# Kernel optimization log

Measured on AMD Instinct MI355X. Metric: run time of the kernel, lower is better.

Reference implementation:

```python
import jax, jax.numpy as jnp
import numpy as np

TEMPERATURE = 1.0  # forward default
INIT_STD = 0.01    # per-class gate init: N(0, 0.01)

def setup_inputs() -> dict:
    key = jax.random.key(0)
    kf, kws, kw1, kw2 = jax.random.split(key, 4)
    B, F, H, C, E = 256, 2048, 512, 512, 8
    Hh = H // 2  # 256
    features = jax.random.normal(kf, (B, F), dtype=jnp.float32)
    # shared transform Linear(F, H) -- default torch init approximated by small normal
    Ws = jax.random.normal(kws, (F, H), dtype=jnp.float32) * (1.0 / np.sqrt(F))
    bs = jnp.zeros((H,), dtype=jnp.float32)
    # per-class gates, stacked over class dim: N(0, 0.01) init, zero bias (as in module)
    W1 = jax.random.normal(kw1, (C, H, Hh), dtype=jnp.float32) * INIT_STD
    b1 = jnp.zeros((C, Hh), dtype=jnp.float32)
    W2 = jax.random.normal(kw2, (C, Hh, E), dtype=jnp.float32) * INIT_STD
    b2 = jnp.zeros((C, E), dtype=jnp.float32)
    return {"features": features, "Ws": Ws, "bs": bs, "W1": W1, "b1": b1, "W2": W2, "b2": b2}

def reference(features, Ws, bs, W1, b1, W2, b2):
    # shared transform: Linear -> ReLU (Dropout is identity at inference)
    shared = jax.nn.relu(features @ Ws + bs)                      # [B, H]
    # batched per-class MLP: one grouped GEMM across all classes
    h = jax.nn.relu(jnp.einsum('bh,chk->bck', shared, W1) + b1)   # [B, C, H/2]
    gate_logits = jnp.einsum('bck,cke->bce', h, W2) + b2          # [B, C, E]
    gate_weights = jax.nn.softmax(gate_logits / TEMPERATURE, axis=-1)
    return (gate_weights, gate_logits)
```

## Files before the change

### kernel.cpp

```cpp
#include <hip/hip_runtime.h>
#include <hip/hip_bf16.h>

#define BATCH 256
#define F_DIM 2048
#define H_DIM 512
#define HH    256
#define NCLS  512
#define E_DIM 8

typedef __attribute__((ext_vector_type(8))) short  bf16x8;
typedef __attribute__((ext_vector_type(4))) float  f32x4;
typedef __attribute__((ext_vector_type(4))) unsigned short u16x4;

__device__ __forceinline__ unsigned short f2bf(float x) {
    union { float f; unsigned int u; } v; v.f = x;
    unsigned int r = v.u + 0x7fffu + ((v.u >> 16) & 1u);
    return (unsigned short)(r >> 16);
}

__global__ __launch_bounds__(256) void k_gemm1(
    const float* __restrict__ features,
    const float* __restrict__ Ws,
    float* __restrict__ partials)
{
    const int tid = threadIdx.x;
    const int lane = tid & 63;
    const int wave = tid >> 6;
    const int job = blockIdx.x * 4 + wave;
    const int kidx = job & 7;
    const int ng  = (job >> 3) & 7;
    const int mt  = job >> 6;
    const int l15 = lane & 15, quad = lane >> 4;
    const int m0 = mt * 16, n0 = ng * 64, kb = kidx * 256;

    f32x4 z = {0.f, 0.f, 0.f, 0.f};
    f32x4 acc[4];
#pragma unroll
    for (int nf = 0; nf < 4; ++nf) acc[nf] = z;

#pragma unroll
    for (int ks = 0; ks < 8; ++ks) {
        const int kk = kb + ks * 32 + quad * 8;
        f32x4 a0 = *(const f32x4*)(features + (size_t)(m0 + l15) * F_DIM + kk);
        f32x4 a1 = *(const f32x4*)(features + (size_t)(m0 + l15) * F_DIM + kk + 4);
        bf16x8 aF;
#pragma unroll
        for (int j = 0; j < 4; ++j) { aF[j] = (short)f2bf(a0[j]); aF[4 + j] = (short)f2bf(a1[j]); }
#pragma unroll
        for (int nf = 0; nf < 4; ++nf) {
            bf16x8 bF;
#pragma unroll
            for (int j = 0; j < 8; ++j)
                bF[j] = (short)f2bf(Ws[(size_t)(kk + j) * H_DIM + n0 + nf * 16 + l15]);
            acc[nf] = __builtin_amdgcn_mfma_f32_16x16x32_bf16(aF, bF, acc[nf], 0, 0, 0);
        }
    }
    float* po = partials + (size_t)kidx * (BATCH * H_DIM);
#pragma unroll
    for (int nf = 0; nf < 4; ++nf)
#pragma unroll
        for (int r = 0; r < 4; ++r)
            po[(size_t)(m0 + quad * 4 + r) * H_DIM + n0 + nf * 16 + l15] = acc[nf][r];
}

__global__ __launch_bounds__(256) void k_reduce_relu(
    const float* __restrict__ partials, const float* __restrict__ bs,
    unsigned short* __restrict__ sharedA)
{
    const int idx = (blockIdx.x * 256 + threadIdx.x) * 4;
    f32x4 s = *(const f32x4*)(partials + idx);
#pragma unroll
    for (int p = 1; p < 8; ++p)
        s += *(const f32x4*)(partials + (size_t)p * (BATCH * H_DIM) + idx);
    s += *(const f32x4*)(bs + (idx & (H_DIM - 1)));
    u16x4 o;
#pragma unroll
    for (int j = 0; j < 4; ++j) {
        float v = s[j] > 0.f ? s[j] : 0.f;
        o[j] = f2bf(v);
    }
    *(u16x4*)(sharedA + idx) = o;
}

__global__ __launch_bounds__(512) void k_main(
    const unsigned short* __restrict__ sharedA,
    const float* __restrict__ W1,
    const float* __restrict__ b1,
    const float* __restrict__ W2,
    const float* __restrict__ b2,
    float* __restrict__ out)
{
    const int c = blockIdx.x;
    const int tid = threadIdx.x;
    const int lane = tid & 63;
    const int wave = tid >> 6;
    const int l15 = lane & 15;
    const int quad = lane >> 4;
    const int g  = wave & 3;
    const int mh = wave >> 2;
    const int n0w = g * 64;
    const int m0w = mh * 128;

    const float* __restrict__ W1c = W1 + (size_t)c * (H_DIM * HH);

    __shared__ float slot[4][BATCH][E_DIM];

    f32x4 z = {0.f, 0.f, 0.f, 0.f};
    f32x4 acc[8][4];
#pragma unroll
    for (int mf = 0; mf < 8; ++mf)
#pragma unroll
        for (int nf = 0; nf < 4; ++nf) acc[mf][nf] = z;

    float braw[2][32];
#pragma unroll
    for (int nf = 0; nf < 4; ++nf)
#pragma unroll
        for (int j = 0; j < 8; ++j)
            braw[0][nf * 8 + j] = W1c[(size_t)(quad * 8 + j) * HH + n0w + nf * 16 + l15];

#pragma unroll
    for (int ks = 0; ks < 16; ++ks) {
        const int cur = ks & 1;
        if (ks < 15) {
            const int k0n = (ks + 1) * 32;
#pragma unroll
            for (int nf = 0; nf < 4; ++nf)
#pragma unroll
                for (int j = 0; j < 8; ++j)
                    braw[cur ^ 1][nf * 8 + j] =
                        W1c[(size_t)(k0n + quad * 8 + j) * HH + n0w + nf * 16 + l15];
        }
        bf16x8 bF[4];
#pragma unroll
        for (int nf = 0; nf < 4; ++nf)
#pragma unroll
            for (int j = 0; j < 8; ++j)
                bF[nf][j] = (short)f2bf(braw[cur][nf * 8 + j]);

        const int k0 = ks * 32 + quad * 8;
#pragma unroll
        for (int mf = 0; mf < 8; ++mf) {
            bf16x8 aF = *(const bf16x8*)(sharedA + (size_t)(m0w + mf * 16 + l15) * H_DIM + k0);
#pragma unroll
            for (int nf = 0; nf < 4; ++nf)
                acc[mf][nf] = __builtin_amdgcn_mfma_f32_16x16x32_bf16(aF, bF[nf], acc[mf][nf], 0, 0, 0);
        }
    }

    float b1v[4];
    f32x4 w2a[4], w2b[4];
#pragma unroll
    for (int nf = 0; nf < 4; ++nf) {
        const int col = n0w + nf * 16 + l15;
        b1v[nf] = b1[(size_t)c * HH + col];
        w2a[nf] = *(const f32x4*)(W2 + ((size_t)c * HH + col) * E_DIM);
        w2b[nf] = *(const f32x4*)(W2 + ((size_t)c * HH + col) * E_DIM + 4);
    }

#pragma unroll
    for (int mf = 0; mf < 8; ++mf) {
        float part[4][E_DIM];
#pragma unroll
        for (int r = 0; r < 4; ++r)
#pragma unroll
            for (int e = 0; e < E_DIM; ++e) part[r][e] = 0.f;
#pragma unroll
        for (int nf = 0; nf < 4; ++nf) {
#pragma unroll
            for (int r = 0; r < 4; ++r) {
                float h = acc[mf][nf][r] + b1v[nf];
                h = h > 0.f ? h : 0.f;
                part[r][0] += h * w2a[nf][0]; part[r][1] += h * w2a[nf][1];
                part[r][2] += h * w2a[nf][2]; part[r][3] += h * w2a[nf][3];
                part[r][4] += h * w2b[nf][0]; part[r][5] += h * w2b[nf][1];
                part[r][6] += h * w2b[nf][2]; part[r][7] += h * w2b[nf][3];
            }
        }
#pragma unroll
        for (int r = 0; r < 4; ++r)
#pragma unroll
            for (int e = 0; e < E_DIM; ++e) {
                float v = part[r][e];
                v += __shfl_xor(v, 1, 16);
                v += __shfl_xor(v, 2, 16);
                v += __shfl_xor(v, 4, 16);
                v += __shfl_xor(v, 8, 16);
                part[r][e] = v;
            }
        if (l15 == 0) {
#pragma unroll
            for (int r = 0; r < 4; ++r) {
                const int row = m0w + mf * 16 + quad * 4 + r;
                f32x4 lo = {part[r][0], part[r][1], part[r][2], part[r][3]};
                f32x4 hi = {part[r][4], part[r][5], part[r][6], part[r][7]};
                *(f32x4*)(&slot[g][row][0]) = lo;
                *(f32x4*)(&slot[g][row][4]) = hi;
            }
        }
    }
    __syncthreads();

    if (tid < BATCH) {
        f32x4 lg0 = *(f32x4*)(&slot[0][tid][0]);
        f32x4 lg1 = *(f32x4*)(&slot[0][tid][4]);
#pragma unroll
        for (int s = 1; s < 4; ++s) {
            lg0 += *(f32x4*)(&slot[s][tid][0]);
            lg1 += *(f32x4*)(&slot[s][tid][4]);
        }
        lg0 += *(const f32x4*)(b2 + (size_t)c * E_DIM);
        lg1 += *(const f32x4*)(b2 + (size_t)c * E_DIM + 4);

        float lg[8] = {lg0[0], lg0[1], lg0[2], lg0[3], lg1[0], lg1[1], lg1[2], lg1[3]};
        float mx = lg[0];
#pragma unroll
        for (int e = 1; e < 8; ++e) mx = lg[e] > mx ? lg[e] : mx;
        float ex[8], s = 0.f;
#pragma unroll
        for (int e = 0; e < 8; ++e) { ex[e] = __expf(lg[e] - mx); s += ex[e]; }
        const float inv = 1.f / s;

        const size_t ob = ((size_t)tid * NCLS + c) * E_DIM;
        f32x4 w0 = {ex[0] * inv, ex[1] * inv, ex[2] * inv, ex[3] * inv};
        f32x4 w1 = {ex[4] * inv, ex[5] * inv, ex[6] * inv, ex[7] * inv};
        *(f32x4*)(out + ob) = w0;
        *(f32x4*)(out + ob + 4) = w1;
        const size_t lbase = (size_t)BATCH * NCLS * E_DIM;
        f32x4 o0 = {lg[0], lg[1], lg[2], lg[3]};
        f32x4 o1 = {lg[4], lg[5], lg[6], lg[7]};
        *(f32x4*)(out + lbase + ob) = o0;
        *(f32x4*)(out + lbase + ob + 4) = o1;
    }
}

extern "C" void kernel_launch(void* const* d_in, const int* in_sizes, int n_in,
                              void* d_out, int out_size, void* d_ws, size_t ws_size,
                              hipStream_t stream) {
    const float* features = (const float*)d_in[0];
    const float* Ws       = (const float*)d_in[1];
    const float* bs       = (const float*)d_in[2];
    const float* W1       = (const float*)d_in[3];
    const float* b1       = (const float*)d_in[4];
    const float* W2       = (const float*)d_in[5];
    const float* b2       = (const float*)d_in[6];
    float* out = (float*)d_out;

    char* ws = (char*)d_ws;
    float*          parts   = (float*)ws;
    unsigned short* sharedA = (unsigned short*)(ws + 4 * 1048576);

    hipLaunchKernelGGL(k_gemm1,       dim3(256), dim3(256), 0, stream, features, Ws, parts);
    hipLaunchKernelGGL(k_reduce_relu, dim3(128), dim3(256), 0, stream, parts, bs, sharedA);
    hipLaunchKernelGGL(k_main,        dim3(NCLS), dim3(512), 0, stream, sharedA, W1, b1, W2, b2, out);
}
```

Before: 471.4 us.

## Split per-class gate GEMM across four column blocks with LDS-staged W1

Each class is now handled by four 256-thread blocks, each covering a 64-column slice of the hidden dimension, which gives 2048 blocks instead of 512 to improve occupancy and latency hiding. W1 is loaded coalesced, converted to bf16 and staged through a double-buffered LDS tile, replacing the strided per-lane register loads. Partial logits go to a workspace buffer, and a separate softmax kernel sums the four partials, adds the bias and writes both outputs. The cost is an extra kernel launch and an 16 MB round-trip of partial logits through global memory, and sharedA is re-read four times per class.

```diff
diff --git a/kernel.cpp b/kernel.cpp
--- a/kernel.cpp
+++ b/kernel.cpp
@@ -82,84 +82,87 @@
     *(u16x4*)(sharedA + idx) = o;
 }
 
-__global__ __launch_bounds__(512) void k_main(
+__global__ __launch_bounds__(256, 3) void k_main(
     const unsigned short* __restrict__ sharedA,
     const float* __restrict__ W1,
     const float* __restrict__ b1,
     const float* __restrict__ W2,
-    const float* __restrict__ b2,
-    float* __restrict__ out)
-{
-    const int c = blockIdx.x;
+    float* __restrict__ part4)
+{
+    const int c = blockIdx.x >> 2;
+    const int q = blockIdx.x & 3;
     const int tid = threadIdx.x;
     const int lane = tid & 63;
     const int wave = tid >> 6;
     const int l15 = lane & 15;
     const int quad = lane >> 4;
-    const int g  = wave & 3;
-    const int mh = wave >> 2;
-    const int n0w = g * 64;
-    const int m0w = mh * 128;
-
-    const float* __restrict__ W1c = W1 + (size_t)c * (H_DIM * HH);
-
-    __shared__ float slot[4][BATCH][E_DIM];
+    const int m0w = wave * 64;
+    const int colL = tid & 63;
+    const int kseg = tid >> 6;
+
+    const float* __restrict__ W1cq = W1 + (size_t)c * (H_DIM * HH) + q * 64;
+
+    __shared__ unsigned short buf[2][8 * 64 * 8];
 
     f32x4 z = {0.f, 0.f, 0.f, 0.f};
-    f32x4 acc[8][4];
-#pragma unroll
-    for (int mf = 0; mf < 8; ++mf)
+    f32x4 acc[4][4];
+#pragma unroll
+    for (int mf = 0; mf < 4; ++mf)
 #pragma unroll
         for (int nf = 0; nf < 4; ++nf) acc[mf][nf] = z;
 
-    float braw[2][32];
-#pragma unroll
-    for (int nf = 0; nf < 4; ++nf)
-#pragma unroll
-        for (int j = 0; j < 8; ++j)
-            braw[0][nf * 8 + j] = W1c[(size_t)(quad * 8 + j) * HH + n0w + nf * 16 + l15];
-
-#pragma unroll
-    for (int ks = 0; ks < 16; ++ks) {
-        const int cur = ks & 1;
-        if (ks < 15) {
-            const int k0n = (ks + 1) * 32;
-#pragma unroll
-            for (int nf = 0; nf < 4; ++nf)
-#pragma unroll
-                for (int j = 0; j < 8; ++j)
-                    braw[cur ^ 1][nf * 8 + j] =
-                        W1c[(size_t)(k0n + quad * 8 + j) * HH + n0w + nf * 16 + l15];
-        }
-        bf16x8 bF[4];
-#pragma unroll
-        for (int nf = 0; nf < 4; ++nf)
-#pragma unroll
-            for (int j = 0; j < 8; ++j)
-                bF[nf][j] = (short)f2bf(braw[cur][nf * 8 + j]);
-
-        const int k0 = ks * 32 + quad * 8;
-#pragma unroll
-        for (int mf = 0; mf < 8; ++mf) {
-            bf16x8 aF = *(const bf16x8*)(sharedA + (size_t)(m0w + mf * 16 + l15) * H_DIM + k0);
-#pragma unroll
-            for (int nf = 0; nf < 4; ++nf)
-                acc[mf][nf] = __builtin_amdgcn_mfma_f32_16x16x32_bf16(aF, bF[nf], acc[mf][nf], 0, 0, 0);
-        }
-    }
-
+    float rg[16];
+#pragma unroll
+    for (int j = 0; j < 16; ++j)
+        rg[j] = W1cq[(size_t)(kseg * 16 + j) * HH + colL];
+
+#pragma unroll
+    for (int ch = 0; ch < 8; ++ch) {
+        unsigned short* bp = &buf[ch & 1][0];
+#pragma unroll
+        for (int h = 0; h < 2; ++h) {
+            bf16x8 v;
+#pragma unroll
+            for (int j = 0; j < 8; ++j) v[j] = (short)f2bf(rg[h * 8 + j]);
+            const int kg = kseg * 2 + h;
+            *(bf16x8*)(bp + ((kg * 64 + colL) << 3)) = v;
+        }
+        __syncthreads();
+        if (ch < 7) {
+#pragma unroll
+            for (int j = 0; j < 16; ++j)
+                rg[j] = W1cq[(size_t)((ch + 1) * 64 + kseg * 16 + j) * HH + colL];
+        }
+#pragma unroll
+        for (int ks = 0; ks < 2; ++ks) {
+            const int k0 = ch * 64 + ks * 32 + quad * 8;
+            bf16x8 aF[4];
+#pragma unroll
+            for (int mf = 0; mf < 4; ++mf)
+                aF[mf] = *(const bf16x8*)(sharedA + (size_t)(m0w + mf * 16 + l15) * H_DIM + k0);
+#pragma unroll
+            for (int nf = 0; nf < 4; ++nf) {
+                bf16x8 bF = *(const bf16x8*)(bp + (((ks * 4 + quad) * 64 + nf * 16 + l15) << 3));
+#pragma unroll
+                for (int mf = 0; mf < 4; ++mf)
+                    acc[mf][nf] = __builtin_amdgcn_mfma_f32_16x16x32_bf16(aF[mf], bF, acc[mf][nf], 0, 0, 0);
+            }
+        }
+    }
+
+    const int cq = q * 64;
     float b1v[4];
     f32x4 w2a[4], w2b[4];
 #pragma unroll
     for (int nf = 0; nf < 4; ++nf) {
-        const int col = n0w + nf * 16 + l15;
+        const int col = cq + nf * 16 + l15;
         b1v[nf] = b1[(size_t)c * HH + col];
         w2a[nf] = *(const f32x4*)(W2 + ((size_t)c * HH + col) * E_DIM);
         w2b[nf] = *(const f32x4*)(W2 + ((size_t)c * HH + col) * E_DIM + 4);
     }
 
 #pragma unroll
-    for (int mf = 0; mf < 8; ++mf) {
+    for (int mf = 0; mf < 4; ++mf) {
         float part[4][E_DIM];
 #pragma unroll
         for (int r = 0; r < 4; ++r)
@@ -194,44 +197,51 @@
                 const int row = m0w + mf * 16 + quad * 4 + r;
                 f32x4 lo = {part[r][0], part[r][1], part[r][2], part[r][3]};
                 f32x4 hi = {part[r][4], part[r][5], part[r][6], part[r][7]};
-                *(f32x4*)(&slot[g][row][0]) = lo;
-                *(f32x4*)(&slot[g][row][4]) = hi;
-            }
-        }
-    }
-    __syncthreads();
-
-    if (tid < BATCH) {
-        f32x4 lg0 = *(f32x4*)(&slot[0][tid][0]);
-        f32x4 lg1 = *(f32x4*)(&slot[0][tid][4]);
-#pragma unroll
-        for (int s = 1; s < 4; ++s) {
-            lg0 += *(f32x4*)(&slot[s][tid][0]);
-            lg1 += *(f32x4*)(&slot[s][tid][4]);
-        }
-        lg0 += *(const f32x4*)(b2 + (size_t)c * E_DIM);
-        lg1 += *(const f32x4*)(b2 + (size_t)c * E_DIM + 4);
-
-        float lg[8] = {lg0[0], lg0[1], lg0[2], lg0[3], lg1[0], lg1[1], lg1[2], lg1[3]};
-        float mx = lg[0];
-#pragma unroll
-        for (int e = 1; e < 8; ++e) mx = lg[e] > mx ? lg[e] : mx;
-        float ex[8], s = 0.f;
-#pragma unroll
-        for (int e = 0; e < 8; ++e) { ex[e] = __expf(lg[e] - mx); s += ex[e]; }
-        const float inv = 1.f / s;
-
-        const size_t ob = ((size_t)tid * NCLS + c) * E_DIM;
-        f32x4 w0 = {ex[0] * inv, ex[1] * inv, ex[2] * inv, ex[3] * inv};
-        f32x4 w1 = {ex[4] * inv, ex[5] * inv, ex[6] * inv, ex[7] * inv};
-        *(f32x4*)(out + ob) = w0;
-        *(f32x4*)(out + ob + 4) = w1;
-        const size_t lbase = (size_t)BATCH * NCLS * E_DIM;
-        f32x4 o0 = {lg[0], lg[1], lg[2], lg[3]};
-        f32x4 o1 = {lg[4], lg[5], lg[6], lg[7]};
-        *(f32x4*)(out + lbase + ob) = o0;
-        *(f32x4*)(out + lbase + ob + 4) = o1;
-    }
+                float* dst = part4 + (((size_t)q * NCLS + c) * BATCH + row) * E_DIM;
+                *(f32x4*)dst = lo;
+                *(f32x4*)(dst + 4) = hi;
+            }
+        }
+    }
+}
+
+__global__ __launch_bounds__(256) void k_softmax(
+    const float* __restrict__ part4,
+    const float* __restrict__ b2,
+    float* __restrict__ out)
+{
+    const int c = blockIdx.x;
+    const int b = threadIdx.x;
+
+    f32x4 lg0 = {0.f, 0.f, 0.f, 0.f}, lg1 = {0.f, 0.f, 0.f, 0.f};
+#pragma unroll
+    for (int qq = 0; qq < 4; ++qq) {
+        const float* p = part4 + (((size_t)qq * NCLS + c) * BATCH + b) * E_DIM;
+        lg0 += *(const f32x4*)p;
+        lg1 += *(const f32x4*)(p + 4);
+    }
+    lg0 += *(const f32x4*)(b2 + (size_t)c * E_DIM);
+    lg1 += *(const f32x4*)(b2 + (size_t)c * E_DIM + 4);
+
+    float lg[8] = {lg0[0], lg0[1], lg0[2], lg0[3], lg1[0], lg1[1], lg1[2], lg1[3]};
+    float mx = lg[0];
+#pragma unroll
+    for (int e = 1; e < 8; ++e) mx = lg[e] > mx ? lg[e] : mx;
+    float ex[8], s = 0.f;
+#pragma unroll
+    for (int e = 0; e < 8; ++e) { ex[e] = __expf(lg[e] - mx); s += ex[e]; }
+    const float inv = 1.f / s;
+
+    const size_t ob = ((size_t)b * NCLS + c) * E_DIM;
+    f32x4 w0 = {ex[0] * inv, ex[1] * inv, ex[2] * inv, ex[3] * inv};
+    f32x4 w1 = {ex[4] * inv, ex[5] * inv, ex[6] * inv, ex[7] * inv};
+    *(f32x4*)(out + ob) = w0;
+    *(f32x4*)(out + ob + 4) = w1;
+    const size_t lbase = (size_t)BATCH * NCLS * E_DIM;
+    f32x4 o0 = {lg[0], lg[1], lg[2], lg[3]};
+    f32x4 o1 = {lg[4], lg[5], lg[6], lg[7]};
+    *(f32x4*)(out + lbase + ob) = o0;
+    *(f32x4*)(out + lbase + ob + 4) = o1;
 }
 
 extern "C" void kernel_launch(void* const* d_in, const int* in_sizes, int n_in,
@@ -248,9 +258,11 @@
 
     char* ws = (char*)d_ws;
     float*          parts   = (float*)ws;
-    unsigned short* sharedA = (unsigned short*)(ws + 4 * 1048576);
-
-    hipLaunchKernelGGL(k_gemm1,       dim3(256), dim3(256), 0, stream, features, Ws, parts);
-    hipLaunchKernelGGL(k_reduce_relu, dim3(128), dim3(256), 0, stream, parts, bs, sharedA);
-    hipLaunchKernelGGL(k_main,        dim3(NCLS), dim3(512), 0, stream, sharedA, W1, b1, W2, b2, out);
-}
+    float*          part4   = (float*)ws;
+    unsigned short* sharedA = (unsigned short*)(ws + 16777216);
+
+    hipLaunchKernelGGL(k_gemm1,       dim3(256),  dim3(256), 0, stream, features, Ws, parts);
+    hipLaunchKernelGGL(k_reduce_relu, dim3(128),  dim3(256), 0, stream, parts, bs, sharedA);
+    hipLaunchKernelGGL(k_main,        dim3(2048), dim3(256), 0, stream, sharedA, W1, b1, W2, part4);
+    hipLaunchKernelGGL(k_softmax,     dim3(NCLS), dim3(256), 0, stream, part4, b2, out);
+}
```

After: 454.9 us. 3.5% less time.
